# Performance work log

Measured on AMD Instinct MI355X. Metric: run time of the kernel, lower is better.

The kernel has to match this reference:

```python
import jax, jax.numpy as jnp
import numpy as np

N_NODES = 50000
N_EDGES = 800000
N_GRAPHS = 128
INPUT_DIM = 64
HIDDEN = 64       # num_heads * dim_per_head = 4 * 16
N_HEADS = 4
DK = HIDDEN // N_HEADS   # 16, per-head key/query dim
DV = HIDDEN // N_HEADS   # 16, per-head value dim
NUM_LAYERS = 4           # -> 3 GIN layers
OUT_DIM = 16
LN_EPS = 1e-5


def layer_norm(x, g, b):
    mu = jnp.mean(x, axis=-1, keepdims=True)
    var = jnp.mean(jnp.square(x - mu), axis=-1, keepdims=True)
    return (x - mu) * jax.lax.rsqrt(var + LN_EPS) * g + b


def sab_block(x, Wq, Wk, Wv, Wo, ln_g, ln_b, add_residual):
    # x: [N, S, D_in]; pre-LN self-attention block (Set Transformer SAB)
    xin = layer_norm(x, ln_g, ln_b)
    q = jnp.einsum('nsd,dhk->nshk', xin, Wq)   # [N,S,H,dk]
    k = jnp.einsum('nsd,dhk->nshk', xin, Wk)
    v = jnp.einsum('nsd,dhk->nshk', xin, Wv)   # [N,S,H,dv]
    scores = jnp.einsum('nqhk,nshk->nhqs', q, k) / jnp.sqrt(jnp.asarray(DK, x.dtype))
    att = jax.nn.softmax(scores, axis=-1)
    o = jnp.einsum('nhqs,nshk->nqhk', att, v)
    o = o.reshape(o.shape[0], o.shape[1], N_HEADS * DV)
    o = o @ Wo                                  # [N,S,dim_out]
    if add_residual:
        o = o + x
    return o


def gin_aggregate(h, src, dst):
    # sum-neighbor aggregation; eps=0, learn_eps=False -> (1+0)*h + sum_nbrs
    msg = jax.ops.segment_sum(h[src], dst, num_segments=N_NODES)
    return h + msg


def setup_inputs() -> dict:
    key = jax.random.key(0)
    ks = jax.random.split(key, 16)
    s = 0.05
    feat = jax.random.normal(ks[0], (N_NODES, 4 * INPUT_DIM), dtype=jnp.float32)
    src = jax.random.randint(ks[1], (N_EDGES,), 0, N_NODES)
    dst = jax.random.randint(ks[2], (N_EDGES,), 0, N_NODES)
    graph_ids = jnp.sort(jax.random.randint(ks[3], (N_NODES,), 0, N_GRAPHS))
    L = NUM_LAYERS - 1  # 3 GIN layers, all same shapes (input_dim == hidden)
    Wq = jax.random.normal(ks[4], (L, HIDDEN, N_HEADS, DK), dtype=jnp.float32) * s
    Wk = jax.random.normal(ks[5], (L, HIDDEN, N_HEADS, DK), dtype=jnp.float32) * s
    Wv = jax.random.normal(ks[6], (L, HIDDEN, N_HEADS, DV), dtype=jnp.float32) * s
    Wo = jax.random.normal(ks[7], (L, N_HEADS * DV, HIDDEN), dtype=jnp.float32) * s
    sab_ln_g = jnp.ones((L, HIDDEN), dtype=jnp.float32)
    sab_ln_b = jnp.zeros((L, HIDDEN), dtype=jnp.float32)
    ln1_g = jnp.ones((L, HIDDEN), dtype=jnp.float32)
    ln1_b = jnp.zeros((L, HIDDEN), dtype=jnp.float32)
    ln2_g = jnp.ones((L, HIDDEN), dtype=jnp.float32)
    ln2_b = jnp.zeros((L, HIDDEN), dtype=jnp.float32)
    W_pred = jax.random.normal(ks[8], (NUM_LAYERS, HIDDEN, OUT_DIM), dtype=jnp.float32) * s
    b_pred = jnp.zeros((NUM_LAYERS, OUT_DIM), dtype=jnp.float32)
    return {"feat": feat, "src": src, "dst": dst, "graph_ids": graph_ids,
            "Wq": Wq, "Wk": Wk, "Wv": Wv, "Wo": Wo,
            "sab_ln_g": sab_ln_g, "sab_ln_b": sab_ln_b,
            "ln1_g": ln1_g, "ln1_b": ln1_b, "ln2_g": ln2_g, "ln2_b": ln2_b,
            "W_pred": W_pred, "b_pred": b_pred}


def reference(feat, src, dst, graph_ids, Wq, Wk, Wv, Wo,
              sab_ln_g, sab_ln_b, ln1_g, ln1_b, ln2_g, ln2_b, W_pred, b_pred):
    h = feat.reshape(N_NODES, -1, INPUT_DIM)   # [N, S, D]
    hidden_rep = [h]
    for i in range(NUM_LAYERS - 1):
        if i == 0:
            agg = gin_aggregate(h, src, dst)
            h = sab_block(agg, Wq[i], Wk[i], Wv[i], Wo[i],
                          sab_ln_g[i], sab_ln_b[i], add_residual=False)
        else:
            h_pre = layer_norm(h, ln1_g[i], ln1_b[i])
            agg = gin_aggregate(h_pre, src, dst)
            h = h + sab_block(agg, Wq[i], Wk[i], Wv[i], Wo[i],
                              sab_ln_g[i], sab_ln_b[i], add_residual=True)
        hidden_rep.append(layer_norm(jax.nn.relu(h), ln2_g[i], ln2_b[i]))
    score = jnp.zeros((N_GRAPHS, hidden_rep[0].shape[1], OUT_DIM), dtype=feat.dtype)
    for i, hh in enumerate(hidden_rep):
        pooled = jax.ops.segment_sum(hh, graph_ids, num_segments=N_GRAPHS)  # [B,S,D]
        score = score + pooled @ W_pred[i] + b_pred[i]
    return score
```

## Files before the change

### kernel.cpp

```cpp
#include <hip/hip_runtime.h>

#define NN 50000
#define NE 800000
#define NG 128
#define RREP 16
#define RSTRIDE 50048

typedef __attribute__((ext_vector_type(8))) short short8;
typedef __attribute__((ext_vector_type(4))) float f32x4;

__device__ __forceinline__ unsigned short f2bf(float f){
  union { float f; unsigned int u; } v; v.f = f;
  return (unsigned short)((v.u + 0x8000u) >> 16);
}
__device__ __forceinline__ float bf2f(unsigned short h){
  union { unsigned int u; float f; } v; v.u = ((unsigned int)h) << 16;
  return v.f;
}

__global__ __launch_bounds__(256) void k_goff(const int* __restrict__ gid,
                                              int* __restrict__ goff){
  int i = blockIdx.x*256 + threadIdx.x;
  if (i >= NN) return;
  int c = gid[i];
  int p = (i == 0) ? -1 : gid[i-1];
  for (int g = p+1; g <= c; ++g) goff[g] = i;
  if (i == NN-1){
    for (int g = c+1; g <= NG; ++g) goff[g] = NN;
  }
}

__global__ __launch_bounds__(256) void k_count_rep(const int* __restrict__ idx,
                                                   int* __restrict__ cnt_rep, int n){
  int i = blockIdx.x*256 + threadIdx.x;
  int r = blockIdx.x & (RREP-1);
  if (i < n) atomicAdd(&cnt_rep[r*RSTRIDE + idx[i]], 1);
}

__global__ __launch_bounds__(256) void k_reduce_rep(const int* __restrict__ cnt_rep,
                                                    int* __restrict__ cnt){
  int i = blockIdx.x*256 + threadIdx.x;
  if (i < NN){
    int s = 0;
    #pragma unroll
    for (int r=0; r<RREP; ++r) s += cnt_rep[r*RSTRIDE + i];
    cnt[i] = s;
  }
}

__global__ __launch_bounds__(256) void k_blocksum(const int* __restrict__ in, int n,
                                                  int* __restrict__ bsum){
  __shared__ int ws4[4];
  int i = blockIdx.x*256 + threadIdx.x;
  int v = (i < n) ? in[i] : 0;
  #pragma unroll
  for (int d=1; d<64; d<<=1) v += __shfl_xor(v, d);
  int lane = threadIdx.x & 63, w = threadIdx.x >> 6;
  if (lane == 0) ws4[w] = v;
  __syncthreads();
  if (threadIdx.x == 0) bsum[blockIdx.x] = ws4[0]+ws4[1]+ws4[2]+ws4[3];
}

__global__ __launch_bounds__(256) void k_scan_small(const int* __restrict__ in, int n,
                                                    int* __restrict__ out){
  __shared__ int wsum[4];
  int tid = threadIdx.x, lane = tid & 63, w = tid >> 6;
  int v = (tid < n) ? in[tid] : 0;
  int x = v;
  #pragma unroll
  for (int d=1; d<64; d<<=1){ int y = __shfl_up(x, d); if (lane >= d) x += y; }
  if (lane == 63) wsum[w] = x;
  __syncthreads();
  int pre2 = 0;
  for (int j=0; j<w; ++j) pre2 += wsum[j];
  int incl = x + pre2;
  if (tid < n) out[tid] = incl - v;
  if (tid == n-1) out[n] = incl;
}

__global__ __launch_bounds__(256) void k_scan_apply(const int* __restrict__ in, int n,
                                                    const int* __restrict__ boff,
                                                    int* __restrict__ out){
  __shared__ int wsum[4];
  int tid = threadIdx.x, lane = tid & 63, w = tid >> 6;
  int i = blockIdx.x*256 + tid;
  int v = (i < n) ? in[i] : 0;
  int x = v;
  #pragma unroll
  for (int d=1; d<64; d<<=1){ int y = __shfl_up(x, d); if (lane >= d) x += y; }
  if (lane == 63) wsum[w] = x;
  __syncthreads();
  int pre2 = boff[blockIdx.x];
  for (int j=0; j<w; ++j) pre2 += wsum[j];
  int excl = x - v + pre2;
  if (i < n){
    out[i] = excl;
    if (i == n-1) out[n] = excl + v;
  }
}

__global__ __launch_bounds__(256) void k_fpos_rep(const int* __restrict__ cnt_rep,
                                                  const int* __restrict__ off,
                                                  int* __restrict__ fpos_rep){
  int i = blockIdx.x*256 + threadIdx.x;
  if (i < NN){
    int p = off[i];
    #pragma unroll
    for (int r=0; r<RREP; ++r){
      fpos_rep[r*RSTRIDE + i] = p;
      p += cnt_rep[r*RSTRIDE + i];
    }
  }
}

__global__ __launch_bounds__(256) void k_fill_rep(const int* __restrict__ src,
                                                  const int* __restrict__ dst,
                                                  int* __restrict__ fpos_rep,
                                                  int* __restrict__ csr, int n){
  int i = blockIdx.x*256 + threadIdx.x;
  int r = blockIdx.x & (RREP-1);
  if (i < n){
    int p = atomicAdd(&fpos_rep[r*RSTRIDE + dst[i]], 1);
    csr[p] = src[i];
  }
}

__global__ __launch_bounds__(256) void k_wt(const float* __restrict__ Wq,
                                            const float* __restrict__ Wk,
                                            const float* __restrict__ Wv,
                                            const float* __restrict__ Wo,
                                            unsigned short* __restrict__ Wt){
  int gid = blockIdx.x*256 + threadIdx.x;
  int l   = gid >> 14;
  int rem = gid & 16383;
  int mat = rem >> 12;
  int idx = rem & 4095;
  int c = idx >> 6, n = idx & 63;
  const float* srcp = (mat==0)?Wq:(mat==1)?Wk:(mat==2)?Wv:Wo;
  float v = srcp[l*4096 + idx];
  Wt[l*16384 + (mat*64 + n)*64 + c] = f2bf(v);
}

__global__ __launch_bounds__(256) void k_f2bf(const float* __restrict__ in,
                                              unsigned short* __restrict__ out){
  int i = blockIdx.x*256 + threadIdx.x;
  float4 v = ((const float4*)in)[i];
  ushort4 o; o.x=f2bf(v.x); o.y=f2bf(v.y); o.z=f2bf(v.z); o.w=f2bf(v.w);
  ((ushort4*)out)[i] = o;
}

__global__ __launch_bounds__(256) void k_layer(const unsigned short* __restrict__ pre_in,
                                               unsigned short* __restrict__ h,
                                               unsigned short* __restrict__ lnout,
                                               unsigned short* __restrict__ pre_next,
                                               const int* __restrict__ off,
                                               const int* __restrict__ csr,
                                               const unsigned short* __restrict__ Wt,
                                               const float* __restrict__ lng,
                                               const float* __restrict__ lnb,
                                               const float* __restrict__ g2,
                                               const float* __restrict__ b2,
                                               const float* __restrict__ g1,
                                               const float* __restrict__ b1,
                                               int residual, int write_pre, int write_h){
  __shared__ unsigned short xo_s[4][16][72];
  __shared__ unsigned short agg_s[4][16][72];
  __shared__ unsigned short qkv_s[4][16][200];

  int tid = threadIdx.x;
  int w = tid >> 6, lane = tid & 63;
  int c16 = lane & 15, kb = lane >> 4;
  int R0 = blockIdx.x*64 + w*16;
  int node0 = blockIdx.x*16 + w*4;

  const ushort4* base = (const ushort4*)pre_in;
  float4 gv = ((const float4*)lng)[c16];
  float4 bv = ((const float4*)lnb)[c16];

  for (int nn=0; nn<4; ++nn){
    int node = node0 + nn;
    int s = off[node], e = off[node+1];
    ushort4 u = base[node*64 + lane];
    float a0 = bf2f(u.x), a1 = bf2f(u.y), a2 = bf2f(u.z), a3 = bf2f(u.w);
    int i = s;
    for (; i + 4 <= e; i += 4){
      int n0 = csr[i], n1 = csr[i+1], n2 = csr[i+2], n3 = csr[i+3];
      ushort4 u0 = base[n0*64 + lane], u1 = base[n1*64 + lane];
      ushort4 u2 = base[n2*64 + lane], u3 = base[n3*64 + lane];
      a0 += bf2f(u0.x)+bf2f(u1.x)+bf2f(u2.x)+bf2f(u3.x);
      a1 += bf2f(u0.y)+bf2f(u1.y)+bf2f(u2.y)+bf2f(u3.y);
      a2 += bf2f(u0.z)+bf2f(u1.z)+bf2f(u2.z)+bf2f(u3.z);
      a3 += bf2f(u0.w)+bf2f(u1.w)+bf2f(u2.w)+bf2f(u3.w);
    }
    for (; i < e; ++i){
      int n0 = csr[i];
      ushort4 u0 = base[n0*64 + lane];
      a0 += bf2f(u0.x); a1 += bf2f(u0.y); a2 += bf2f(u0.z); a3 += bf2f(u0.w);
    }
    int m = nn*4 + kb;
    if (residual){
      ushort4 o; o.x=f2bf(a0); o.y=f2bf(a1); o.z=f2bf(a2); o.w=f2bf(a3);
      *(ushort4*)&agg_s[w][m][c16*4] = o;
    }
    float s0 = a0+a1+a2+a3;
    float q0 = a0*a0+a1*a1+a2*a2+a3*a3;
    #pragma unroll
    for (int d=1; d<16; d<<=1){ s0 += __shfl_xor(s0, d); q0 += __shfl_xor(q0, d); }
    float mu = s0*(1.f/64.f);
    float rs = rsqrtf(q0*(1.f/64.f) - mu*mu + 1e-5f);
    ushort4 o;
    o.x=f2bf((a0-mu)*rs*gv.x+bv.x); o.y=f2bf((a1-mu)*rs*gv.y+bv.y);
    o.z=f2bf((a2-mu)*rs*gv.z+bv.z); o.w=f2bf((a3-mu)*rs*gv.w+bv.w);
    *(ushort4*)&xo_s[w][m][c16*4] = o;
  }

  short8 a0v = *(const short8*)&xo_s[w][c16][kb*8];
  short8 a1v = *(const short8*)&xo_s[w][c16][32 + kb*8];
  f32x4 acc[12];
  #pragma unroll
  for (int t=0; t<12; ++t){
    short8 b0 = *(const short8*)&Wt[(t*16 + c16)*64 + kb*8];
    short8 b1 = *(const short8*)&Wt[(t*16 + c16)*64 + 32 + kb*8];
    f32x4 z = {0.f, 0.f, 0.f, 0.f};
    z = __builtin_amdgcn_mfma_f32_16x16x32_bf16(a0v, b0, z, 0, 0, 0);
    z = __builtin_amdgcn_mfma_f32_16x16x32_bf16(a1v, b1, z, 0, 0, 0);
    acc[t] = z;
  }
  #pragma unroll
  for (int t=0; t<12; ++t){
    #pragma unroll
    for (int r=0; r<4; ++r)
      qkv_s[w][kb*4 + r][t*16 + c16] = f2bf(acc[t][r]);
  }

  {
    int p = lane >> 2, qr = lane & 3;
    int ns = p >> 2, hd = p & 3;
    int mrow = ns*4 + qr;
    int qc = hd*16, kc = 64 + hd*16, vc = 128 + hd*16;
    float qv[16];
    short8 u0 = *(const short8*)&qkv_s[w][mrow][qc];
    short8 u1 = *(const short8*)&qkv_s[w][mrow][qc+8];
    #pragma unroll
    for (int j=0; j<8; ++j){
      qv[j]   = bf2f((unsigned short)u0[j]);
      qv[8+j] = bf2f((unsigned short)u1[j]);
    }
    float sc[4];
    #pragma unroll
    for (int kr=0; kr<4; ++kr){
      short8 k0 = *(const short8*)&qkv_s[w][ns*4+kr][kc];
      short8 k1 = *(const short8*)&qkv_s[w][ns*4+kr][kc+8];
      float d2 = 0.f;
      #pragma unroll
      for (int j=0; j<8; ++j){
        d2 += qv[j]  *bf2f((unsigned short)k0[j]);
        d2 += qv[8+j]*bf2f((unsigned short)k1[j]);
      }
      sc[kr] = d2 * 0.25f;
    }
    float mx = fmaxf(fmaxf(sc[0],sc[1]), fmaxf(sc[2],sc[3]));
    float e0=__expf(sc[0]-mx), e1=__expf(sc[1]-mx), e2=__expf(sc[2]-mx), e3=__expf(sc[3]-mx);
    float inv = 1.f/(e0+e1+e2+e3);
    float at[4] = {e0*inv, e1*inv, e2*inv, e3*inv};
    float ov[16];
    #pragma unroll
    for (int j=0; j<16; ++j) ov[j] = 0.f;
    #pragma unroll
    for (int kr=0; kr<4; ++kr){
      short8 v0 = *(const short8*)&qkv_s[w][ns*4+kr][vc];
      short8 v1 = *(const short8*)&qkv_s[w][ns*4+kr][vc+8];
      #pragma unroll
      for (int j=0; j<8; ++j){
        ov[j]   += at[kr]*bf2f((unsigned short)v0[j]);
        ov[8+j] += at[kr]*bf2f((unsigned short)v1[j]);
      }
    }
    short8 s0v, s1v;
    #pragma unroll
    for (int j=0; j<8; ++j){
      s0v[j] = (short)f2bf(ov[j]);
      s1v[j] = (short)f2bf(ov[8+j]);
    }
    *(short8*)&xo_s[w][mrow][qc]   = s0v;
    *(short8*)&xo_s[w][mrow][qc+8] = s1v;
  }

  {
    short8 oa0 = *(const short8*)&xo_s[w][c16][kb*8];
    short8 oa1 = *(const short8*)&xo_s[w][c16][32 + kb*8];
    #pragma unroll
    for (int t=0; t<4; ++t){
      short8 b0 = *(const short8*)&Wt[(192 + t*16 + c16)*64 + kb*8];
      short8 b1 = *(const short8*)&Wt[(192 + t*16 + c16)*64 + 32 + kb*8];
      f32x4 z = {0.f, 0.f, 0.f, 0.f};
      z = __builtin_amdgcn_mfma_f32_16x16x32_bf16(oa0, b0, z, 0, 0, 0);
      z = __builtin_amdgcn_mfma_f32_16x16x32_bf16(oa1, b1, z, 0, 0, 0);
      #pragma unroll
      for (int r=0; r<4; ++r)
        xo_s[w][kb*4 + r][t*16 + c16] = f2bf(z[r]);
    }
  }

  float4 g2v = ((const float4*)g2)[c16];
  float4 b2v = ((const float4*)b2)[c16];
  float4 g1v, b1v;
  if (write_pre){ g1v = ((const float4*)g1)[c16]; b1v = ((const float4*)b1)[c16]; }
  #pragma unroll
  for (int rr=0; rr<4; ++rr){
    int m = rr*4 + kb;
    int row = R0 + m;
    ushort4 uv = *(const ushort4*)&xo_s[w][m][c16*4];
    float v0 = bf2f(uv.x), v1 = bf2f(uv.y), v2 = bf2f(uv.z), v3 = bf2f(uv.w);
    if (residual){
      ushort4 hh = ((const ushort4*)h)[row*16 + c16];
      ushort4 ag = *(const ushort4*)&agg_s[w][m][c16*4];
      v0 += bf2f(hh.x) + bf2f(ag.x);
      v1 += bf2f(hh.y) + bf2f(ag.y);
      v2 += bf2f(hh.z) + bf2f(ag.z);
      v3 += bf2f(hh.w) + bf2f(ag.w);
    }
    float r0 = fmaxf(v0,0.f), r1 = fmaxf(v1,0.f), r2 = fmaxf(v2,0.f), r3 = fmaxf(v3,0.f);
    float s1 = v0+v1+v2+v3, q1 = v0*v0+v1*v1+v2*v2+v3*v3;
    float s2 = r0+r1+r2+r3, q2 = r0*r0+r1*r1+r2*r2+r3*r3;
    #pragma unroll
    for (int d=1; d<16; d<<=1){
      s1 += __shfl_xor(s1, d); q1 += __shfl_xor(q1, d);
      s2 += __shfl_xor(s2, d); q2 += __shfl_xor(q2, d);
    }
    float mu1 = s1*(1.f/64.f), rs1 = rsqrtf(q1*(1.f/64.f) - mu1*mu1 + 1e-5f);
    float mu2 = s2*(1.f/64.f), rs2 = rsqrtf(q2*(1.f/64.f) - mu2*mu2 + 1e-5f);
    if (write_h){
      ushort4 o; o.x=f2bf(v0); o.y=f2bf(v1); o.z=f2bf(v2); o.w=f2bf(v3);
      ((ushort4*)h)[row*16 + c16] = o;
    }
    {
      ushort4 o;
      o.x=f2bf((r0-mu2)*rs2*g2v.x+b2v.x); o.y=f2bf((r1-mu2)*rs2*g2v.y+b2v.y);
      o.z=f2bf((r2-mu2)*rs2*g2v.z+b2v.z); o.w=f2bf((r3-mu2)*rs2*g2v.w+b2v.w);
      ((ushort4*)lnout)[row*16 + c16] = o;
    }
    if (write_pre){
      ushort4 o;
      o.x=f2bf((v0-mu1)*rs1*g1v.x+b1v.x); o.y=f2bf((v1-mu1)*rs1*g1v.y+b1v.y);
      o.z=f2bf((v2-mu1)*rs1*g1v.z+b1v.z); o.w=f2bf((v3-mu1)*rs1*g1v.w+b1v.w);
      ((ushort4*)pre_next)[row*16 + c16] = o;
    }
  }
}

__global__ __launch_bounds__(256) void k_pool8(const float* __restrict__ src,
                                               const int* __restrict__ goff,
                                               float* __restrict__ out){
  int g = blockIdx.x >> 3, sub = blockIdx.x & 7, t = threadIdx.x;
  int s = goff[g], e = goff[g+1], len = e - s;
  int s0 = s + ((len*sub) >> 3), e0 = s + ((len*(sub+1)) >> 3);
  float a0=0.f, a1=0.f;
  int n = s0;
  for (; n + 2 <= e0; n += 2){ a0 += src[n*256 + t]; a1 += src[(n+1)*256 + t]; }
  if (n < e0) a0 += src[n*256 + t];
  atomicAdd(&out[g*256 + t], a0 + a1);
}

__global__ __launch_bounds__(256) void k_pool8b(const unsigned short* __restrict__ src,
                                                const int* __restrict__ goff,
                                                float* __restrict__ out){
  int g = blockIdx.x >> 3, sub = blockIdx.x & 7, t = threadIdx.x;
  int s = goff[g], e = goff[g+1], len = e - s;
  int s0 = s + ((len*sub) >> 3), e0 = s + ((len*(sub+1)) >> 3);
  float a0=0.f, a1=0.f;
  int n = s0;
  for (; n + 2 <= e0; n += 2){ a0 += bf2f(src[n*256 + t]); a1 += bf2f(src[(n+1)*256 + t]); }
  if (n < e0) a0 += bf2f(src[n*256 + t]);
  atomicAdd(&out[g*256 + t], a0 + a1);
}

__global__ __launch_bounds__(256) void k_final(const float* __restrict__ pooled,
                                               const float* __restrict__ Wp,
                                               const float* __restrict__ bp,
                                               float* __restrict__ out){
  int t = blockIdx.x*256 + threadIdx.x;
  int b = t >> 6, s = (t >> 4) & 3, o = t & 15;
  float acc = 0.f;
  for (int i=0; i<4; ++i){
    acc += bp[i*16 + o];
    const float* pr = pooled + i*32768 + b*256 + s*64;
    const float* wp = Wp + i*1024 + o;
    float a = 0.f;
    #pragma unroll 8
    for (int c=0; c<64; ++c) a += pr[c]*wp[c*16];
    acc += a;
  }
  out[t] = acc;
}

static const size_t OFF_H     = 0;
static const size_t OFF_LNOUT = 25600000;
static const size_t OFF_PRE0  = 51200000;
static const size_t OFF_PRE1  = 76800000;
static const size_t OFF_CSR   = 102400000;
static const size_t OFF_CNT   = 105600000;
static const size_t OFF_OFF   = 105800064;
static const size_t OFF_GOFF  = 106000128;
static const size_t OFF_POOL  = 106000704;
static const size_t OFF_WT    = 106525056;
static const size_t OFF_BSUM  = 106623360;
static const size_t OFF_BOFF  = 106624192;

extern "C" void kernel_launch(void* const* d_in, const int* in_sizes, int n_in,
                              void* d_out, int out_size, void* d_ws, size_t ws_size,
                              hipStream_t stream) {
  const float* feat = (const float*)d_in[0];
  const int*   src  = (const int*)d_in[1];
  const int*   dst  = (const int*)d_in[2];
  const int*   gid  = (const int*)d_in[3];
  const float* Wq   = (const float*)d_in[4];
  const float* Wk   = (const float*)d_in[5];
  const float* Wv   = (const float*)d_in[6];
  const float* Wo   = (const float*)d_in[7];
  const float* sg   = (const float*)d_in[8];
  const float* sb   = (const float*)d_in[9];
  const float* l1g  = (const float*)d_in[10];
  const float* l1b  = (const float*)d_in[11];
  const float* l2g  = (const float*)d_in[12];
  const float* l2b  = (const float*)d_in[13];
  const float* Wp   = (const float*)d_in[14];
  const float* bp   = (const float*)d_in[15];
  float* out = (float*)d_out;

  char* ws = (char*)d_ws;
  unsigned short* h      = (unsigned short*)(ws + OFF_H);
  unsigned short* lnout  = (unsigned short*)(ws + OFF_LNOUT);
  unsigned short* pre0   = (unsigned short*)(ws + OFF_PRE0);
  unsigned short* pre1   = (unsigned short*)(ws + OFF_PRE1);
  int*            csr    = (int*)(ws + OFF_CSR);
  int*            cnt    = (int*)(ws + OFF_CNT);
  int*            off    = (int*)(ws + OFF_OFF);
  int*            goff   = (int*)(ws + OFF_GOFF);
  float*          pooled = (float*)(ws + OFF_POOL);
  unsigned short* Wt     = (unsigned short*)(ws + OFF_WT);
  int*            bsum   = (int*)(ws + OFF_BSUM);
  int*            boff   = (int*)(ws + OFF_BOFF);
  int*            cnt_rep  = (int*)(ws + OFF_H);
  int*            fpos_rep = (int*)(ws + OFF_H + (size_t)RREP*RSTRIDE*4);

  hipMemsetAsync(cnt_rep, 0, (size_t)RREP*RSTRIDE*4, stream);
  hipMemsetAsync(pooled, 0, 4*NG*256*sizeof(float), stream);

  k_count_rep<<<NE/256, 256, 0, stream>>>(dst, cnt_rep, NE);
  k_goff<<<(NN+255)/256, 256, 0, stream>>>(gid, goff);
  k_reduce_rep<<<(NN+255)/256, 256, 0, stream>>>(cnt_rep, cnt);
  k_blocksum<<<196, 256, 0, stream>>>(cnt, NN, bsum);
  k_scan_small<<<1, 256, 0, stream>>>(bsum, 196, boff);
  k_scan_apply<<<196, 256, 0, stream>>>(cnt, NN, boff, off);
  k_fpos_rep<<<(NN+255)/256, 256, 0, stream>>>(cnt_rep, off, fpos_rep);
  k_fill_rep<<<NE/256, 256, 0, stream>>>(src, dst, fpos_rep, csr, NE);

  k_wt<<<192, 256, 0, stream>>>(Wq, Wk, Wv, Wo, Wt);
  k_f2bf<<<12500, 256, 0, stream>>>(feat, pre0);
  k_pool8<<<NG*8, 256, 0, stream>>>(feat, goff, pooled + 0*32768);

  k_layer<<<3125, 256, 0, stream>>>(pre0, h, lnout, pre1, off, csr, Wt + 0*16384,
                                    sg + 0, sb + 0, l2g + 0, l2b + 0,
                                    l1g + 1*64, l1b + 1*64, 0, 1, 1);
  k_pool8b<<<NG*8, 256, 0, stream>>>(lnout, goff, pooled + 1*32768);

  k_layer<<<3125, 256, 0, stream>>>(pre1, h, lnout, pre0, off, csr, Wt + 1*16384,
                                    sg + 1*64, sb + 1*64, l2g + 1*64, l2b + 1*64,
                                    l1g + 2*64, l1b + 2*64, 1, 1, 1);
  k_pool8b<<<NG*8, 256, 0, stream>>>(lnout, goff, pooled + 2*32768);

  k_layer<<<3125, 256, 0, stream>>>(pre0, h, lnout, pre1, off, csr, Wt + 2*16384,
                                    sg + 2*64, sb + 2*64, l2g + 2*64, l2b + 2*64,
                                    l1g + 2*64, l1b + 2*64, 1, 0, 0);
  k_pool8b<<<NG*8, 256, 0, stream>>>(lnout, goff, pooled + 3*32768);

  k_final<<<32, 256, 0, stream>>>(pooled, Wp, bp, out);
}
```

Measured before the change: 683.5 us.

## Split GIN aggregation into chunk-major gather kernel separate from SAB kernel

Stores the pre-aggregation node features in a chunk-major layout (8 slices of 32 features per node) and runs the neighbor gather as its own kernel, with one grid dimension per feature chunk. Each chunk slice is about 3.2 MB, small enough to stay cache-resident while the random neighbor gathers run, instead of gathering whole 512-byte rows from a 25.6 MB array. The SAB/attention kernel then reads the aggregated rows from a new workspace buffer. This adds an extra write and read of the full aggregate per layer and an extra launch, and each random neighbor now costs eight 64-byte gathers instead of one 512-byte one.

```diff
diff --git a/kernel.cpp b/kernel.cpp
--- a/kernel.cpp
+++ b/kernel.cpp
@@ -141,28 +141,60 @@
   Wt[l*16384 + (mat*64 + n)*64 + c] = f2bf(v);
 }
 
-__global__ __launch_bounds__(256) void k_f2bf(const float* __restrict__ in,
-                                              unsigned short* __restrict__ out){
+__global__ __launch_bounds__(256) void k_f2bf_c(const float* __restrict__ in,
+                                                unsigned short* __restrict__ out){
   int i = blockIdx.x*256 + threadIdx.x;
   float4 v = ((const float4*)in)[i];
   ushort4 o; o.x=f2bf(v.x); o.y=f2bf(v.y); o.z=f2bf(v.z); o.w=f2bf(v.w);
-  ((ushort4*)out)[i] = o;
-}
-
-__global__ __launch_bounds__(256) void k_layer(const unsigned short* __restrict__ pre_in,
-                                               unsigned short* __restrict__ h,
-                                               unsigned short* __restrict__ lnout,
-                                               unsigned short* __restrict__ pre_next,
+  int flat = i << 2;
+  int node = flat >> 8, f = flat & 255;
+  int chunk = f >> 5;
+  ((ushort4*)out)[(size_t)chunk*NN*8 + node*8 + ((f & 31) >> 2)] = o;
+}
+
+__global__ __launch_bounds__(256) void k_agg_c(const unsigned short* __restrict__ pre_c,
                                                const int* __restrict__ off,
                                                const int* __restrict__ csr,
-                                               const unsigned short* __restrict__ Wt,
-                                               const float* __restrict__ lng,
-                                               const float* __restrict__ lnb,
-                                               const float* __restrict__ g2,
-                                               const float* __restrict__ b2,
-                                               const float* __restrict__ g1,
-                                               const float* __restrict__ b1,
-                                               int residual, int write_pre, int write_h){
+                                               unsigned short* __restrict__ agg){
+  int chunk = blockIdx.y;
+  int w = threadIdx.x >> 6, lane = threadIdx.x & 63;
+  int lg = lane >> 3, li = lane & 7;
+  int node = (blockIdx.x*4 + w)*8 + lg;
+  if (node >= NN) return;
+  const ushort4* slice = (const ushort4*)pre_c + (size_t)chunk*NN*8;
+  int s = off[node], e = off[node+1];
+  ushort4 u = slice[node*8 + li];
+  float a0 = bf2f(u.x), a1 = bf2f(u.y), a2 = bf2f(u.z), a3 = bf2f(u.w);
+  int i = s;
+  for (; i + 2 <= e; i += 2){
+    int n0 = csr[i], n1 = csr[i+1];
+    ushort4 u0 = slice[n0*8 + li], u1 = slice[n1*8 + li];
+    a0 += bf2f(u0.x)+bf2f(u1.x);
+    a1 += bf2f(u0.y)+bf2f(u1.y);
+    a2 += bf2f(u0.z)+bf2f(u1.z);
+    a3 += bf2f(u0.w)+bf2f(u1.w);
+  }
+  if (i < e){
+    int n0 = csr[i];
+    ushort4 u0 = slice[n0*8 + li];
+    a0 += bf2f(u0.x); a1 += bf2f(u0.y); a2 += bf2f(u0.z); a3 += bf2f(u0.w);
+  }
+  ushort4 o; o.x=f2bf(a0); o.y=f2bf(a1); o.z=f2bf(a2); o.w=f2bf(a3);
+  ((ushort4*)agg)[node*64 + chunk*8 + li] = o;
+}
+
+__global__ __launch_bounds__(256) void k_sab(const unsigned short* __restrict__ agg,
+                                             unsigned short* __restrict__ h,
+                                             unsigned short* __restrict__ lnout,
+                                             unsigned short* __restrict__ pre_next,
+                                             const unsigned short* __restrict__ Wt,
+                                             const float* __restrict__ lng,
+                                             const float* __restrict__ lnb,
+                                             const float* __restrict__ g2,
+                                             const float* __restrict__ b2,
+                                             const float* __restrict__ g1,
+                                             const float* __restrict__ b1,
+                                             int residual, int write_pre, int write_h){
   __shared__ unsigned short xo_s[4][16][72];
   __shared__ unsigned short agg_s[4][16][72];
   __shared__ unsigned short qkv_s[4][16][200];
@@ -171,47 +203,27 @@
   int w = tid >> 6, lane = tid & 63;
   int c16 = lane & 15, kb = lane >> 4;
   int R0 = blockIdx.x*64 + w*16;
-  int node0 = blockIdx.x*16 + w*4;
-
-  const ushort4* base = (const ushort4*)pre_in;
-  float4 gv = ((const float4*)lng)[c16];
-  float4 bv = ((const float4*)lnb)[c16];
-
-  for (int nn=0; nn<4; ++nn){
-    int node = node0 + nn;
-    int s = off[node], e = off[node+1];
-    ushort4 u = base[node*64 + lane];
-    float a0 = bf2f(u.x), a1 = bf2f(u.y), a2 = bf2f(u.z), a3 = bf2f(u.w);
-    int i = s;
-    for (; i + 4 <= e; i += 4){
-      int n0 = csr[i], n1 = csr[i+1], n2 = csr[i+2], n3 = csr[i+3];
-      ushort4 u0 = base[n0*64 + lane], u1 = base[n1*64 + lane];
-      ushort4 u2 = base[n2*64 + lane], u3 = base[n3*64 + lane];
-      a0 += bf2f(u0.x)+bf2f(u1.x)+bf2f(u2.x)+bf2f(u3.x);
-      a1 += bf2f(u0.y)+bf2f(u1.y)+bf2f(u2.y)+bf2f(u3.y);
-      a2 += bf2f(u0.z)+bf2f(u1.z)+bf2f(u2.z)+bf2f(u3.z);
-      a3 += bf2f(u0.w)+bf2f(u1.w)+bf2f(u2.w)+bf2f(u3.w);
-    }
-    for (; i < e; ++i){
-      int n0 = csr[i];
-      ushort4 u0 = base[n0*64 + lane];
-      a0 += bf2f(u0.x); a1 += bf2f(u0.y); a2 += bf2f(u0.z); a3 += bf2f(u0.w);
-    }
-    int m = nn*4 + kb;
-    if (residual){
-      ushort4 o; o.x=f2bf(a0); o.y=f2bf(a1); o.z=f2bf(a2); o.w=f2bf(a3);
-      *(ushort4*)&agg_s[w][m][c16*4] = o;
-    }
-    float s0 = a0+a1+a2+a3;
-    float q0 = a0*a0+a1*a1+a2*a2+a3*a3;
-    #pragma unroll
-    for (int d=1; d<16; d<<=1){ s0 += __shfl_xor(s0, d); q0 += __shfl_xor(q0, d); }
-    float mu = s0*(1.f/64.f);
-    float rs = rsqrtf(q0*(1.f/64.f) - mu*mu + 1e-5f);
-    ushort4 o;
-    o.x=f2bf((a0-mu)*rs*gv.x+bv.x); o.y=f2bf((a1-mu)*rs*gv.y+bv.y);
-    o.z=f2bf((a2-mu)*rs*gv.z+bv.z); o.w=f2bf((a3-mu)*rs*gv.w+bv.w);
-    *(ushort4*)&xo_s[w][m][c16*4] = o;
+
+  {
+    float4 gv = ((const float4*)lng)[c16];
+    float4 bv = ((const float4*)lnb)[c16];
+    #pragma unroll
+    for (int rr=0; rr<4; ++rr){
+      int m = rr*4 + kb;
+      ushort4 uv = ((const ushort4*)agg)[(R0+m)*16 + c16];
+      if (residual) *(ushort4*)&agg_s[w][m][c16*4] = uv;
+      float vx = bf2f(uv.x), vy = bf2f(uv.y), vz = bf2f(uv.z), vw = bf2f(uv.w);
+      float s = vx+vy+vz+vw;
+      float q = vx*vx+vy*vy+vz*vz+vw*vw;
+      #pragma unroll
+      for (int d=1; d<16; d<<=1){ s += __shfl_xor(s, d); q += __shfl_xor(q, d); }
+      float mu = s*(1.f/64.f);
+      float rs = rsqrtf(q*(1.f/64.f) - mu*mu + 1e-5f);
+      ushort4 o;
+      o.x=f2bf((vx-mu)*rs*gv.x+bv.x); o.y=f2bf((vy-mu)*rs*gv.y+bv.y);
+      o.z=f2bf((vz-mu)*rs*gv.z+bv.z); o.w=f2bf((vw-mu)*rs*gv.w+bv.w);
+      *(ushort4*)&xo_s[w][m][c16*4] = o;
+    }
   }
 
   short8 a0v = *(const short8*)&xo_s[w][c16][kb*8];
@@ -341,10 +353,13 @@
       ((ushort4*)lnout)[row*16 + c16] = o;
     }
     if (write_pre){
+      int nd = row >> 2;
+      int f = (row & 3)*64 + 4*c16;
+      int chunk = f >> 5;
       ushort4 o;
       o.x=f2bf((v0-mu1)*rs1*g1v.x+b1v.x); o.y=f2bf((v1-mu1)*rs1*g1v.y+b1v.y);
       o.z=f2bf((v2-mu1)*rs1*g1v.z+b1v.z); o.w=f2bf((v3-mu1)*rs1*g1v.w+b1v.w);
-      ((ushort4*)pre_next)[row*16 + c16] = o;
+      ((ushort4*)pre_next)[(size_t)chunk*NN*8 + nd*8 + ((f & 31) >> 2)] = o;
     }
   }
 }
@@ -398,14 +413,15 @@
 static const size_t OFF_LNOUT = 25600000;
 static const size_t OFF_PRE0  = 51200000;
 static const size_t OFF_PRE1  = 76800000;
-static const size_t OFF_CSR   = 102400000;
-static const size_t OFF_CNT   = 105600000;
-static const size_t OFF_OFF   = 105800064;
-static const size_t OFF_GOFF  = 106000128;
-static const size_t OFF_POOL  = 106000704;
-static const size_t OFF_WT    = 106525056;
-static const size_t OFF_BSUM  = 106623360;
-static const size_t OFF_BOFF  = 106624192;
+static const size_t OFF_AGG   = 102400000;
+static const size_t OFF_CSR   = 128000000;
+static const size_t OFF_CNT   = 131200000;
+static const size_t OFF_OFF   = 131400064;
+static const size_t OFF_GOFF  = 131600128;
+static const size_t OFF_POOL  = 131600704;
+static const size_t OFF_WT    = 132124992;
+static const size_t OFF_BSUM  = 132223296;
+static const size_t OFF_BOFF  = 132224128;
 
 extern "C" void kernel_launch(void* const* d_in, const int* in_sizes, int n_in,
                               void* d_out, int out_size, void* d_ws, size_t ws_size,
@@ -433,6 +449,7 @@
   unsigned short* lnout  = (unsigned short*)(ws + OFF_LNOUT);
   unsigned short* pre0   = (unsigned short*)(ws + OFF_PRE0);
   unsigned short* pre1   = (unsigned short*)(ws + OFF_PRE1);
+  unsigned short* agg    = (unsigned short*)(ws + OFF_AGG);
   int*            csr    = (int*)(ws + OFF_CSR);
   int*            cnt    = (int*)(ws + OFF_CNT);
   int*            off    = (int*)(ws + OFF_OFF);
@@ -457,22 +474,27 @@
   k_fill_rep<<<NE/256, 256, 0, stream>>>(src, dst, fpos_rep, csr, NE);
 
   k_wt<<<192, 256, 0, stream>>>(Wq, Wk, Wv, Wo, Wt);
-  k_f2bf<<<12500, 256, 0, stream>>>(feat, pre0);
+  k_f2bf_c<<<12500, 256, 0, stream>>>(feat, pre0);
   k_pool8<<<NG*8, 256, 0, stream>>>(feat, goff, pooled + 0*32768);
 
-  k_layer<<<3125, 256, 0, stream>>>(pre0, h, lnout, pre1, off, csr, Wt + 0*16384,
-                                    sg + 0, sb + 0, l2g + 0, l2b + 0,
-                                    l1g + 1*64, l1b + 1*64, 0, 1, 1);
+  dim3 aggGrid(1563, 8);
+
+  k_agg_c<<<aggGrid, 256, 0, stream>>>(pre0, off, csr, agg);
+  k_sab<<<3125, 256, 0, stream>>>(agg, h, lnout, pre1, Wt + 0*16384,
+                                  sg + 0, sb + 0, l2g + 0, l2b + 0,
+                                  l1g + 1*64, l1b + 1*64, 0, 1, 1);
   k_pool8b<<<NG*8, 256, 0, stream>>>(lnout, goff, pooled + 1*32768);
 
-  k_layer<<<3125, 256, 0, stream>>>(pre1, h, lnout, pre0, off, csr, Wt + 1*16384,
-                                    sg + 1*64, sb + 1*64, l2g + 1*64, l2b + 1*64,
-                                    l1g + 2*64, l1b + 2*64, 1, 1, 1);
+  k_agg_c<<<aggGrid, 256, 0, stream>>>(pre1, off, csr, agg);
+  k_sab<<<3125, 256, 0, stream>>>(agg, h, lnout, pre0, Wt + 1*16384,
+                                  sg + 1*64, sb + 1*64, l2g + 1*64, l2b + 1*64,
+                                  l1g + 2*64, l1b + 2*64, 1, 1, 1);
   k_pool8b<<<NG*8, 256, 0, stream>>>(lnout, goff, pooled + 2*32768);
 
-  k_layer<<<3125, 256, 0, stream>>>(pre0, h, lnout, pre1, off, csr, Wt + 2*16384,
-                                    sg + 2*64, sb + 2*64, l2g + 2*64, l2b + 2*64,
-                                    l1g + 2*64, l1b + 2*64, 1, 0, 0);
+  k_agg_c<<<aggGrid, 256, 0, stream>>>(pre0, off, csr, agg);
+  k_sab<<<3125, 256, 0, stream>>>(agg, h, lnout, pre1, Wt + 2*16384,
+                                  sg + 2*64, sb + 2*64, l2g + 2*64, l2b + 2*64,
+                                  l1g + 2*64, l1b + 2*64, 1, 0, 0);
   k_pool8b<<<NG*8, 256, 0, stream>>>(lnout, goff, pooled + 3*32768);
 
   k_final<<<32, 256, 0, stream>>>(pooled, Wp, bp, out);
```

Measured after the change: 694.1 us. No clear change (+1.6%).
